# Kernel tuning notes

Measured on AMD Instinct MI355X. Metric: run time of the kernel, lower is better.

The kernel has to match this reference:

```python
import jax, jax.numpy as jnp
import numpy as np

B, N, D = 16, 2048, 512   # batch, tokens, latent dim
K = 8192                  # codebook size


def setup_inputs() -> dict:
    key = jax.random.key(0)
    k1, k2 = jax.random.split(key)
    ze = jax.random.normal(k1, (B, N, D), dtype=jnp.float32)
    codebook = jax.random.normal(k2, (K, D), dtype=jnp.float32)
    return {"ze": ze, "codebook": codebook}


def reference(ze, codebook):
    # Pairwise squared distances: ||ze||^2 + ||c||^2 - 2 ze.c  -> [B, N, K]
    sq_norm = (
        jnp.sum(ze ** 2, axis=-1, keepdims=True)
        + jnp.sum(codebook ** 2, axis=1)
        - 2.0 * jnp.einsum("bnd,kd->bnk", ze, codebook)
    )
    argmin = jnp.argmin(sq_norm, axis=-1)  # [B, N]
    zq = codebook[argmin]                  # gather -> [B, N, D]
    return zq
```

## Files before the change

kernel.cpp:

```cpp
#include <hip/hip_runtime.h>
#include <cfloat>

#define TOKENS 32768
#define DDIM   512
#define KCODES 8192

#define CAP    160
#define MARGIN 2.0f

#define ZEBF_OFF   0
#define CBBF_OFF   (TOKENS * DDIM * 2)
#define CNORM_OFF  (CBBF_OFF + KCODES * DDIM * 2)
#define CNT_OFF    (CNORM_OFF + KCODES * 4)
#define CANDI_OFF  (CNT_OFF + TOKENS * 4)
#define CANDS_OFF  (CANDI_OFF + TOKENS * CAP * 4)
#define WS_REQ     ((size_t)(CANDS_OFF + TOKENS * CAP * 4))

typedef short bf16x8 __attribute__((ext_vector_type(8)));
typedef float f32x4  __attribute__((ext_vector_type(4)));

__device__ __forceinline__ void gld16(const void* g, void* l) {
    __builtin_amdgcn_global_load_lds(
        (const __attribute__((address_space(1))) void*)g,
        (__attribute__((address_space(3))) void*)l,
        16, 0, 0);
}

__device__ __forceinline__ unsigned short f2bf(float f) {
    union { float f; unsigned int u; } v; v.f = f;
    unsigned int u = v.u;
    return (unsigned short)((u + 0x7fffu + ((u >> 16) & 1u)) >> 16);
}

__global__ __launch_bounds__(256) void convert_kernel(const float* __restrict__ src,
                                                      unsigned short* __restrict__ dst,
                                                      int n8) {
    int i = blockIdx.x * 256 + threadIdx.x;
    if (i >= n8) return;
    float4 a = ((const float4*)src)[i * 2];
    float4 b = ((const float4*)src)[i * 2 + 1];
    bf16x8 o;
    o[0] = (short)f2bf(a.x); o[1] = (short)f2bf(a.y);
    o[2] = (short)f2bf(a.z); o[3] = (short)f2bf(a.w);
    o[4] = (short)f2bf(b.x); o[5] = (short)f2bf(b.y);
    o[6] = (short)f2bf(b.z); o[7] = (short)f2bf(b.w);
    *(bf16x8*)&dst[(size_t)i * 8] = o;
}

__global__ __launch_bounds__(256) void cnorm_kernel(const float* __restrict__ cb,
                                                    float* __restrict__ cnorm) {
    int row  = blockIdx.x * 4 + (threadIdx.x >> 6);
    int lane = threadIdx.x & 63;
    const float* r = cb + (size_t)row * DDIM;
    float s = 0.f;
    #pragma unroll
    for (int d = lane; d < DDIM; d += 64) { float v = r[d]; s += v * v; }
    #pragma unroll
    for (int off = 32; off > 0; off >>= 1) s += __shfl_down(s, off, 64);
    if (lane == 0) cnorm[row] = s;
}

__global__ __launch_bounds__(256, 2) void vq_mfma_kernel(
        const unsigned short* __restrict__ zebf,
        const unsigned short* __restrict__ cbbf,
        const float* __restrict__ cnorm,
        int* __restrict__ cnt,
        int* __restrict__ candI,
        float* __restrict__ candS) {
    __shared__ unsigned short Ab[256 * 64];
    __shared__ unsigned short Bb[128 * 64];

    const int tid  = threadIdx.x;
    const int w    = tid >> 6;
    const int lane = tid & 63;

    const int bid      = blockIdx.x;
    const int xcd      = bid & 7;
    const int loc      = bid >> 3;
    const int panel    = loc >> 7;
    const int l2i      = loc & 127;
    const int tb_local = l2i >> 3;
    const int cb_local = l2i & 7;
    const int token_blk = tb_local * 8 + xcd;
    const int code_blk  = panel * 8 + cb_local;

    const int tok0  = token_blk * 256;
    const int code0 = code_blk * 128;

    f32x4 acc[4][8];
    const f32x4 zero = {0.f, 0.f, 0.f, 0.f};
    #pragma unroll
    for (int i = 0; i < 4; ++i)
        #pragma unroll
        for (int j = 0; j < 8; ++j) acc[i][j] = zero;

    for (int dk = 0; dk < DDIM; dk += 64) {
        __syncthreads();
        #pragma unroll
        for (int i = 0; i < 8; ++i) {
            int L    = ((i * 4 + w) * 1024) + lane * 16;
            int row  = L >> 7;
            int phys = (L >> 4) & 7;
            int slog = phys ^ (row & 7);
            gld16(zebf + (size_t)(tok0 + row) * DDIM + dk + slog * 8, (char*)Ab + L);
            if (i < 4)
                gld16(cbbf + (size_t)(code0 + row) * DDIM + dk + slog * 8, (char*)Bb + L);
        }
        __syncthreads();

        #pragma unroll
        for (int kk = 0; kk < 2; ++kk) {
            bf16x8 af[4], bfr[8];
            int slog = kk * 4 + (lane >> 4);
            #pragma unroll
            for (int rt = 0; rt < 4; ++rt) {
                int row  = w * 64 + rt * 16 + (lane & 15);
                int phys = slog ^ (row & 7);
                af[rt] = *(const bf16x8*)(Ab + row * 64 + phys * 8);
            }
            #pragma unroll
            for (int ct = 0; ct < 8; ++ct) {
                int row  = ct * 16 + (lane & 15);
                int phys = slog ^ (row & 7);
                bfr[ct] = *(const bf16x8*)(Bb + row * 64 + phys * 8);
            }
            #pragma unroll
            for (int rt = 0; rt < 4; ++rt)
                #pragma unroll
                for (int ct = 0; ct < 8; ++ct)
                    acc[rt][ct] = __builtin_amdgcn_mfma_f32_16x16x32_bf16(
                        af[rt], bfr[ct], acc[rt][ct], 0, 0, 0);
        }
    }

    float cn[8];
    #pragma unroll
    for (int ct = 0; ct < 8; ++ct)
        cn[ct] = cnorm[code0 + ct * 16 + (lane & 15)];

    #pragma unroll
    for (int rt = 0; rt < 4; ++rt)
        #pragma unroll
        for (int r = 0; r < 4; ++r) {
            float m = cn[0] - 2.f * acc[rt][0][r];
            #pragma unroll
            for (int ct = 1; ct < 8; ++ct)
                m = fminf(m, cn[ct] - 2.f * acc[rt][ct][r]);
            #pragma unroll
            for (int off = 1; off < 16; off <<= 1)
                m = fminf(m, __shfl_xor(m, off, 64));
            float thr = m + MARGIN;

            int token = tok0 + w * 64 + rt * 16 + (lane >> 4) * 4 + r;
            #pragma unroll
            for (int ct = 0; ct < 8; ++ct) {
                float s = cn[ct] - 2.f * acc[rt][ct][r];
                if (s <= thr) {
                    int pos = atomicAdd(&cnt[token], 1);
                    if (pos < CAP) {
                        candI[(size_t)token * CAP + pos] = code0 + ct * 16 + (lane & 15);
                        candS[(size_t)token * CAP + pos] = s;
                    }
                }
            }
        }
}

__global__ __launch_bounds__(64) void rescore_kernel(
        const float* __restrict__ ze, const float* __restrict__ cb,
        const float* __restrict__ cnorm, const int* __restrict__ cnt,
        const int* __restrict__ candI, const float* __restrict__ candS,
        float* __restrict__ out) {
    const int t    = blockIdx.x;
    const int lane = threadIdx.x;

    float4 za = *(const float4*)&ze[(size_t)t * DDIM + lane * 8];
    float4 zb = *(const float4*)&ze[(size_t)t * DDIM + lane * 8 + 4];

    int n = cnt[t];
    bool ovf = (n > CAP) || (n <= 0);

    float best = FLT_MAX;
    int   bidx = 0x7fffffff;

    if (!ovf) {
        float m = FLT_MAX;
        for (int e = lane; e < n; e += 64)
            m = fminf(m, candS[(size_t)t * CAP + e]);
        #pragma unroll
        for (int off = 32; off > 0; off >>= 1)
            m = fminf(m, __shfl_xor(m, off, 64));
        float thr = m + MARGIN;

        for (int base = 0; base < n; base += 64) {
            int e = base + lane;
            int myI = 0; float sv = FLT_MAX;
            if (e < n) { myI = candI[(size_t)t * CAP + e]; sv = candS[(size_t)t * CAP + e]; }
            unsigned long long mask = __ballot(e < n && sv <= thr);
            while (mask) {
                int b = __ffsll((long long)mask) - 1;
                mask &= mask - 1;
                int code = __shfl(myI, b, 64);
                const float* row = cb + (size_t)code * DDIM + lane * 8;
                float4 ca = *(const float4*)row;
                float4 cc = *(const float4*)(row + 4);
                float d = za.x*ca.x + za.y*ca.y + za.z*ca.z + za.w*ca.w
                        + zb.x*cc.x + zb.y*cc.y + zb.z*cc.z + zb.w*cc.w;
                #pragma unroll
                for (int off = 32; off > 0; off >>= 1) d += __shfl_xor(d, off, 64);
                float s = cnorm[code] - 2.f * d;
                if (s < best || (s == best && code < bidx)) { best = s; bidx = code; }
            }
        }
    } else {
        for (int code = 0; code < KCODES; ++code) {
            const float* row = cb + (size_t)code * DDIM + lane * 8;
            float4 ca = *(const float4*)row;
            float4 cc = *(const float4*)(row + 4);
            float d = za.x*ca.x + za.y*ca.y + za.z*ca.z + za.w*ca.w
                    + zb.x*cc.x + zb.y*cc.y + zb.z*cc.z + zb.w*cc.w;
            #pragma unroll
            for (int off = 32; off > 0; off >>= 1) d += __shfl_xor(d, off, 64);
            float s = cnorm[code] - 2.f * d;
            if (s < best || (s == best && code < bidx)) { best = s; bidx = code; }
        }
    }

    const float* src = cb + (size_t)bidx * DDIM + lane * 8;
    float4 o0 = *(const float4*)src;
    float4 o1 = *(const float4*)(src + 4);
    *(float4*)&out[(size_t)t * DDIM + lane * 8]     = o0;
    *(float4*)&out[(size_t)t * DDIM + lane * 8 + 4] = o1;
}

#define TM 64
#define TN 64
#define BK 32
#define LDS_STRIDE (TM + 4)

__global__ __launch_bounds__(256) void vq_fallback_kernel(const float* __restrict__ ze,
                                                          const float* __restrict__ cb,
                                                          const float* __restrict__ cnorm,
                                                          float* __restrict__ out) {
    __shared__ float At[BK][LDS_STRIDE];
    __shared__ float Bt[BK][LDS_STRIDE];
    __shared__ float rv[TM][16];
    __shared__ int   ri[TM][16];
    __shared__ int   best_s[TM];

    const int tid = threadIdx.x;
    const int tx  = tid & 15;
    const int ty  = tid >> 4;
    const int token_base = blockIdx.x * TM;
    const int sc = tid & 31;
    const int sr = tid >> 5;

    float bestv[4] = {FLT_MAX, FLT_MAX, FLT_MAX, FLT_MAX};
    int   besti[4] = {0, 0, 0, 0};

    for (int ctile = 0; ctile < KCODES; ctile += TN) {
        float acc[4][4] = {{0.f}};
        for (int dk = 0; dk < DDIM; dk += BK) {
            __syncthreads();
            #pragma unroll
            for (int p = 0; p < 8; ++p) {
                int r = p * 8 + sr;
                At[sc][r] = ze[(size_t)(token_base + r) * DDIM + dk + sc];
                Bt[sc][r] = cb[(size_t)(ctile + r) * DDIM + dk + sc];
            }
            __syncthreads();
            #pragma unroll
            for (int d = 0; d < BK; ++d) {
                float a[4], b[4];
                *(float4*)a = *(const float4*)&At[d][ty * 4];
                *(float4*)b = *(const float4*)&Bt[d][tx * 4];
                #pragma unroll
                for (int i = 0; i < 4; ++i)
                    #pragma unroll
                    for (int j = 0; j < 4; ++j)
                        acc[i][j] += a[i] * b[j];
            }
        }
        #pragma unroll
        for (int j = 0; j < 4; ++j) {
            int code = ctile + tx * 4 + j;
            float cnv = cnorm[code];
            #pragma unroll
            for (int i = 0; i < 4; ++i) {
                float s = cnv - 2.f * acc[i][j];
                if (s < bestv[i]) { bestv[i] = s; besti[i] = code; }
            }
        }
    }
    #pragma unroll
    for (int i = 0; i < 4; ++i) {
        rv[ty * 4 + i][tx] = bestv[i];
        ri[ty * 4 + i][tx] = besti[i];
    }
    __syncthreads();
    if (tid < TM) {
        float bv = rv[tid][0]; int bi = ri[tid][0];
        #pragma unroll
        for (int x = 1; x < 16; ++x) {
            float v = rv[tid][x]; int ix = ri[tid][x];
            if (v < bv || (v == bv && ix < bi)) { bv = v; bi = ix; }
        }
        best_s[tid] = bi;
    }
    __syncthreads();
    const int gr   = tid >> 7;
    const int gcol = (tid & 127) * 4;
    for (int rr = 0; rr < TM; rr += 2) {
        int tk  = rr + gr;
        int src = best_s[tk];
        float4 v = *(const float4*)&cb[(size_t)src * DDIM + gcol];
        *(float4*)&out[(size_t)(token_base + tk) * DDIM + gcol] = v;
    }
}

extern "C" void kernel_launch(void* const* d_in, const int* in_sizes, int n_in,
                              void* d_out, int out_size, void* d_ws, size_t ws_size,
                              hipStream_t stream) {
    const float* ze = (const float*)d_in[0];
    const float* cb = (const float*)d_in[1];
    float* out      = (float*)d_out;

    if (ws_size < WS_REQ) {
        float* cnorm = (float*)d_ws;
        cnorm_kernel<<<KCODES / 4, 256, 0, stream>>>(cb, cnorm);
        vq_fallback_kernel<<<TOKENS / TM, 256, 0, stream>>>(ze, cb, cnorm, out);
        return;
    }

    char* ws = (char*)d_ws;
    unsigned short* zebf = (unsigned short*)(ws + ZEBF_OFF);
    unsigned short* cbbf = (unsigned short*)(ws + CBBF_OFF);
    float* cnorm = (float*)(ws + CNORM_OFF);
    int*   cnt   = (int*)(ws + CNT_OFF);
    int*   candI = (int*)(ws + CANDI_OFF);
    float* candS = (float*)(ws + CANDS_OFF);

    convert_kernel<<<(TOKENS * DDIM / 8) / 256, 256, 0, stream>>>(ze, zebf, TOKENS * DDIM / 8);
    convert_kernel<<<(KCODES * DDIM / 8) / 256, 256, 0, stream>>>(cb, cbbf, KCODES * DDIM / 8);
    cnorm_kernel<<<KCODES / 4, 256, 0, stream>>>(cb, cnorm);
    hipMemsetAsync(cnt, 0, TOKENS * sizeof(int), stream);

    vq_mfma_kernel<<<(TOKENS / 256) * (KCODES / 128), 256, 0, stream>>>(
        zebf, cbbf, cnorm, cnt, candI, candS);

    rescore_kernel<<<TOKENS, 64, 0, stream>>>(ze, cb, cnorm, cnt, candI, candS, out);
}
```

Before: 772.2 us.

## Shrink MFMA tile to 128x128 with 2x2 wave grid and shared row minima

Shrinks the block tile from 256 tokens x 128 codes to 128x128 and arranges the four waves as a 2x2 grid, each computing 64x64. This cuts LDS per block and the accumulator registers per wave, so the occupancy hint rises from 2 to 3 blocks. Row minima are now combined across the two column waves through shared memory before thresholding. Global-load offsets are precomputed and the LDS fragment addresses use an XOR on kk. In exchange, arithmetic intensity per block drops and the grid doubles, adding more global traffic and an extra barrier.

```diff
diff --git a/kernel.cpp b/kernel.cpp
--- a/kernel.cpp
+++ b/kernel.cpp
@@ -60,105 +60,133 @@
     if (lane == 0) cnorm[row] = s;
 }
 
-__global__ __launch_bounds__(256, 2) void vq_mfma_kernel(
+__global__ __launch_bounds__(256, 3) void vq_mfma_kernel(
         const unsigned short* __restrict__ zebf,
         const unsigned short* __restrict__ cbbf,
         const float* __restrict__ cnorm,
         int* __restrict__ cnt,
         int* __restrict__ candI,
         float* __restrict__ candS) {
-    __shared__ unsigned short Ab[256 * 64];
+    __shared__ unsigned short Ab[128 * 64];
     __shared__ unsigned short Bb[128 * 64];
+    __shared__ float smin[2][128];
 
     const int tid  = threadIdx.x;
     const int w    = tid >> 6;
     const int lane = tid & 63;
+    const int wr   = w >> 1;
+    const int wc   = w & 1;
 
     const int bid      = blockIdx.x;
     const int xcd      = bid & 7;
     const int loc      = bid >> 3;
-    const int panel    = loc >> 7;
-    const int l2i      = loc & 127;
+    const int panel    = loc >> 8;
+    const int l2i      = loc & 255;
     const int tb_local = l2i >> 3;
     const int cb_local = l2i & 7;
     const int token_blk = tb_local * 8 + xcd;
     const int code_blk  = panel * 8 + cb_local;
 
-    const int tok0  = token_blk * 256;
+    const int tok0  = token_blk * 128;
     const int code0 = code_blk * 128;
 
-    f32x4 acc[4][8];
+    int ldsOff[4], offA[4], offB[4];
+    #pragma unroll
+    for (int i = 0; i < 4; ++i) {
+        int L    = ((i * 4 + w) * 1024) + lane * 16;
+        int row  = L >> 7;
+        int phys = (L >> 4) & 7;
+        int slog = phys ^ (row & 7);
+        ldsOff[i] = L;
+        offA[i] = (tok0 + row) * DDIM + slog * 8;
+        offB[i] = (code0 + row) * DDIM + slog * 8;
+    }
+
+    const int s0 = lane >> 4;
+    int aOff[4], bOff[4];
+    #pragma unroll
+    for (int rt = 0; rt < 4; ++rt) {
+        int row  = wr * 64 + rt * 16 + (lane & 15);
+        aOff[rt] = row * 128 + ((s0 ^ (row & 7)) * 16);
+    }
+    #pragma unroll
+    for (int ct = 0; ct < 4; ++ct) {
+        int row  = wc * 64 + ct * 16 + (lane & 15);
+        bOff[ct] = row * 128 + ((s0 ^ (row & 7)) * 16);
+    }
+
+    f32x4 acc[4][4];
     const f32x4 zero = {0.f, 0.f, 0.f, 0.f};
     #pragma unroll
     for (int i = 0; i < 4; ++i)
         #pragma unroll
-        for (int j = 0; j < 8; ++j) acc[i][j] = zero;
+        for (int j = 0; j < 4; ++j) acc[i][j] = zero;
 
     for (int dk = 0; dk < DDIM; dk += 64) {
         __syncthreads();
         #pragma unroll
-        for (int i = 0; i < 8; ++i) {
-            int L    = ((i * 4 + w) * 1024) + lane * 16;
-            int row  = L >> 7;
-            int phys = (L >> 4) & 7;
-            int slog = phys ^ (row & 7);
-            gld16(zebf + (size_t)(tok0 + row) * DDIM + dk + slog * 8, (char*)Ab + L);
-            if (i < 4)
-                gld16(cbbf + (size_t)(code0 + row) * DDIM + dk + slog * 8, (char*)Bb + L);
+        for (int i = 0; i < 4; ++i) {
+            gld16(zebf + (size_t)(offA[i] + dk), (char*)Ab + ldsOff[i]);
+            gld16(cbbf + (size_t)(offB[i] + dk), (char*)Bb + ldsOff[i]);
         }
         __syncthreads();
 
         #pragma unroll
         for (int kk = 0; kk < 2; ++kk) {
-            bf16x8 af[4], bfr[8];
-            int slog = kk * 4 + (lane >> 4);
-            #pragma unroll
-            for (int rt = 0; rt < 4; ++rt) {
-                int row  = w * 64 + rt * 16 + (lane & 15);
-                int phys = slog ^ (row & 7);
-                af[rt] = *(const bf16x8*)(Ab + row * 64 + phys * 8);
-            }
-            #pragma unroll
-            for (int ct = 0; ct < 8; ++ct) {
-                int row  = ct * 16 + (lane & 15);
-                int phys = slog ^ (row & 7);
-                bfr[ct] = *(const bf16x8*)(Bb + row * 64 + phys * 8);
-            }
+            bf16x8 af[4], bfr[4];
+            #pragma unroll
+            for (int rt = 0; rt < 4; ++rt)
+                af[rt] = *(const bf16x8*)((const char*)Ab + (aOff[rt] ^ (kk * 64)));
+            #pragma unroll
+            for (int ct = 0; ct < 4; ++ct)
+                bfr[ct] = *(const bf16x8*)((const char*)Bb + (bOff[ct] ^ (kk * 64)));
             #pragma unroll
             for (int rt = 0; rt < 4; ++rt)
                 #pragma unroll
-                for (int ct = 0; ct < 8; ++ct)
+                for (int ct = 0; ct < 4; ++ct)
                     acc[rt][ct] = __builtin_amdgcn_mfma_f32_16x16x32_bf16(
                         af[rt], bfr[ct], acc[rt][ct], 0, 0, 0);
         }
     }
 
-    float cn[8];
-    #pragma unroll
-    for (int ct = 0; ct < 8; ++ct)
-        cn[ct] = cnorm[code0 + ct * 16 + (lane & 15)];
-
+    float cn[4];
+    #pragma unroll
+    for (int ct = 0; ct < 4; ++ct)
+        cn[ct] = cnorm[code0 + wc * 64 + ct * 16 + (lane & 15)];
+
+    float rm[4][4];
     #pragma unroll
     for (int rt = 0; rt < 4; ++rt)
         #pragma unroll
         for (int r = 0; r < 4; ++r) {
             float m = cn[0] - 2.f * acc[rt][0][r];
             #pragma unroll
-            for (int ct = 1; ct < 8; ++ct)
+            for (int ct = 1; ct < 4; ++ct)
                 m = fminf(m, cn[ct] - 2.f * acc[rt][ct][r]);
             #pragma unroll
             for (int off = 1; off < 16; off <<= 1)
                 m = fminf(m, __shfl_xor(m, off, 64));
-            float thr = m + MARGIN;
-
-            int token = tok0 + w * 64 + rt * 16 + (lane >> 4) * 4 + r;
-            #pragma unroll
-            for (int ct = 0; ct < 8; ++ct) {
+            rm[rt][r] = m;
+            if ((lane & 15) == 0)
+                smin[wc][wr * 64 + rt * 16 + (lane >> 4) * 4 + r] = m;
+        }
+    __syncthreads();
+
+    #pragma unroll
+    for (int rt = 0; rt < 4; ++rt)
+        #pragma unroll
+        for (int r = 0; r < 4; ++r) {
+            int tl = wr * 64 + rt * 16 + (lane >> 4) * 4 + r;
+            float mo  = smin[1 - wc][tl];
+            float thr = fminf(rm[rt][r], mo) + MARGIN;
+            int token = tok0 + tl;
+            #pragma unroll
+            for (int ct = 0; ct < 4; ++ct) {
                 float s = cn[ct] - 2.f * acc[rt][ct][r];
                 if (s <= thr) {
                     int pos = atomicAdd(&cnt[token], 1);
                     if (pos < CAP) {
-                        candI[(size_t)token * CAP + pos] = code0 + ct * 16 + (lane & 15);
+                        candI[(size_t)token * CAP + pos] = code0 + wc * 64 + ct * 16 + (lane & 15);
                         candS[(size_t)token * CAP + pos] = s;
                     }
                 }
@@ -345,7 +373,7 @@
     cnorm_kernel<<<KCODES / 4, 256, 0, stream>>>(cb, cnorm);
     hipMemsetAsync(cnt, 0, TOKENS * sizeof(int), stream);
 
-    vq_mfma_kernel<<<(TOKENS / 256) * (KCODES / 128), 256, 0, stream>>>(
+    vq_mfma_kernel<<<(TOKENS / 128) * (KCODES / 128), 256, 0, stream>>>(
         zebf, cbbf, cnorm, cnt, candI, candS);
 
     rescore_kernel<<<TOKENS, 64, 0, stream>>>(ze, cb, cnorm, cnt, candI, candS, out);
```

Measured after the change: 732.0 us. -5.2%, faster.
